# Optimization experiments

Measured on AMD Instinct MI355X. Metric: run time of the kernel, lower is better.

The kernel has to match this reference:

```python
import jax, jax.numpy as jnp
import numpy as np
import math

# Static config (mirrors init_kwargs)
E, B, S, D, F, HMAX = 8, 4, 1024, 1024, 4096, 8
W = 768                      # active slimmable width (multiple giving integer head_dim)
H = max(1, W * HMAX // D)    # = 6 heads at width 768
HD = W // H                  # = 128
TOPK = 2
EPS = 1e-6


def setup_inputs() -> dict:
    key = jax.random.key(0)
    ks = jax.random.split(key, 14)
    sd = 1.0 / math.sqrt(D)
    sf = 1.0 / math.sqrt(F)
    return {
        "x":  jax.random.normal(ks[0], (B, S, D), jnp.float32),
        "wr": jax.random.normal(ks[1], (D, E), jnp.float32) * sd,
        "qw": jax.random.normal(ks[2], (E, D, D), jnp.float32) * sd,
        "qb": jax.random.normal(ks[3], (E, D), jnp.float32) * sd,
        "kw": jax.random.normal(ks[4], (E, D, D), jnp.float32) * sd,
        "kb": jax.random.normal(ks[5], (E, D), jnp.float32) * sd,
        "vw": jax.random.normal(ks[6], (E, D, D), jnp.float32) * sd,
        "vb": jax.random.normal(ks[7], (E, D), jnp.float32) * sd,
        "ow": jax.random.normal(ks[8], (E, D, D), jnp.float32) * sd,
        "ob": jax.random.normal(ks[9], (E, D), jnp.float32) * sd,
        "w1": jax.random.normal(ks[10], (E, F, D), jnp.float32) * sd,
        "b1": jax.random.normal(ks[11], (E, F), jnp.float32) * sd,
        "w2": jax.random.normal(ks[12], (E, D, F), jnp.float32) * sf,
        "b2": jax.random.normal(ks[13], (E, D), jnp.float32) * sf,
    }


def _slim_linear(x, w, b, in_w, out_w):
    # SlimmableLinear: dynamically slice max-size weight/bias to active widths
    return x @ w[:out_w, :in_w].T + b[:out_w]


def _rms_norm(x):
    # SlimmableExpert._layer_norm: RMS normalization (no mean-subtract, no affine)
    var = jnp.mean(jnp.square(x), axis=-1, keepdims=True)
    return x / jnp.sqrt(var + EPS)


def _expert_fwd(x_s, qw, qb, kw, kb, vw, vb, ow, ob, w1, b1, w2, b2):
    # x_s: [B, S, W]  (already sliced to active width)
    # --- slimmable self-attention at width W ---
    q = _slim_linear(x_s, qw, qb, W, W).reshape(B, S, H, HD).transpose(0, 2, 1, 3)
    k = _slim_linear(x_s, kw, kb, W, W).reshape(B, S, H, HD).transpose(0, 2, 1, 3)
    v = _slim_linear(x_s, vw, vb, W, W).reshape(B, S, H, HD).transpose(0, 2, 1, 3)
    scores = jnp.einsum('bhqd,bhkd->bhqk', q, k) / math.sqrt(HD)   # [B,H,S,S]
    attn = jax.nn.softmax(scores, axis=-1)
    ao = jnp.einsum('bhqk,bhkd->bhqd', attn, v)
    ao = ao.transpose(0, 2, 1, 3).reshape(B, S, W)
    ao = _slim_linear(ao, ow, ob, W, W)
    x1 = _rms_norm(x_s + ao)
    # --- slimmable FFN: W -> F (full) -> W, exact GELU (torch default) ---
    h = jax.nn.gelu(_slim_linear(x1, w1, b1, W, F), approximate=False)
    f = _slim_linear(h, w2, b2, F, W)
    return _rms_norm(x1 + f)   # [B,S,W]


def reference(x, wr, qw, qb, kw, kb, vw, vb, ow, ob, w1, b1, w2, b2):
    # Router: softmax over experts, top-k dispatch with renormalized gates
    logits = jnp.einsum('bsd,de->bse', x, wr)            # [B,S,E]
    probs = jax.nn.softmax(logits, axis=-1)
    topv, topi = jax.lax.top_k(probs, TOPK)              # [B,S,K]
    topv = topv / jnp.sum(topv, axis=-1, keepdims=True)
    bi = jnp.arange(B)[:, None, None]
    si = jnp.arange(S)[None, :, None]
    gate = jnp.zeros((B, S, E), x.dtype).at[bi, si, topi].set(topv)  # sparse gate

    # Slice tokens to active width (width embedding skipped: closest stored
    # width 736 != 768, per source shape-match check)
    x_s = x[..., :W]
    outs = []
    for e in range(E):   # small fixed expert count; bounds peak memory
        outs.append(_expert_fwd(x_s, qw[e], qb[e], kw[e], kb[e], vw[e], vb[e],
                                ow[e], ob[e], w1[e], b1[e], w2[e], b2[e]))
    eo = jnp.stack(outs, axis=0)                          # [E,B,S,W]
    out_w = jnp.einsum('bse,ebsw->bsw', gate, eo)         # gate-weighted combine
    # Zero-pad sliced width back to full model dim (per SlimmableExpert)
    out = jnp.concatenate(
        [out_w, jnp.zeros((B, S, D - W), x.dtype)], axis=-1)
    return out
```

## Files before the change

kernel.cpp:

```cpp
#include <hip/hip_runtime.h>
#include <cstdint>

#define NE 8
#define NB 4
#define NS 1024
#define ND 1024
#define NF 4096
#define NW 768
#define NH 6
#define NHD 128
#define NTOK 4096
#define NBH 24
#define RCAP 10496
#define VSTRIDE ((size_t)NTOK * NW)
#define EPS 1e-6f

typedef unsigned short ush;
typedef __attribute__((ext_vector_type(8))) short short8;
typedef __attribute__((ext_vector_type(4))) float f32x4;
typedef __attribute__((ext_vector_type(4))) unsigned short u16x4;

typedef const __attribute__((address_space(1))) void gvoid_t;
typedef __attribute__((address_space(3))) void lvoid_t;

__device__ __forceinline__ void gload16(const void* g, void* l) {
  __builtin_amdgcn_global_load_lds((gvoid_t*)g, (lvoid_t*)l, 16, 0, 0);
}

__device__ __forceinline__ ush f2b(float f) {
  union { float f; uint32_t u; } x; x.f = f;
  uint32_t r = x.u + 0x7fffu + ((x.u >> 16) & 1u);
  return (ush)(r >> 16);
}
__device__ __forceinline__ float b2f(ush u) {
  union { uint32_t u; float f; } x; x.u = (uint32_t)u << 16;
  return x.f;
}
__device__ __forceinline__ int prefix_sum(const int* __restrict__ c, int n) {
  int s = 0;
#pragma unroll 1
  for (int i = 0; i < n; ++i) s += c[i];
  return s;
}


__global__ __launch_bounds__(256, 4)
void router_kernel(const float* __restrict__ x, const float* __restrict__ wr,
                   float* __restrict__ gate, int* __restrict__ inv) {
  int lane = threadIdx.x & 63, wave = threadIdx.x >> 6;
  int t = blockIdx.x * 4 + wave;
  float acc[NE] = {};
  for (int i = 0; i < 16; ++i) {
    int d = lane + i * 64;
    float xv = x[(size_t)t * ND + d];
    const float* wp = wr + (size_t)d * NE;
    float4 w0 = *(const float4*)wp, w1 = *(const float4*)(wp + 4);
    acc[0] += xv * w0.x; acc[1] += xv * w0.y; acc[2] += xv * w0.z; acc[3] += xv * w0.w;
    acc[4] += xv * w1.x; acc[5] += xv * w1.y; acc[6] += xv * w1.z; acc[7] += xv * w1.w;
  }
#pragma unroll
  for (int e = 0; e < NE; ++e)
    for (int m = 1; m < 64; m <<= 1) acc[e] += __shfl_xor(acc[e], m);
  int i1 = 0; float v1 = acc[0];
#pragma unroll
  for (int e = 1; e < NE; ++e) if (acc[e] > v1) { v1 = acc[e]; i1 = e; }
  int i2 = -1; float v2 = -3.0e38f;
#pragma unroll
  for (int e = 0; e < NE; ++e) if (e != i1 && acc[e] > v2) { v2 = acc[e]; i2 = e; }
  float p2 = __expf(v2 - v1);
  float g1 = 1.0f / (1.0f + p2), g2 = p2 / (1.0f + p2);
  if (lane < NE)
    gate[(size_t)t * NE + lane] = (lane == i1) ? g1 : ((lane == i2) ? g2 : 0.0f);
  if (lane < 2) inv[t * 2 + lane] = -1;
}

__global__ __launch_bounds__(1024, 1)
void build_index(const float* __restrict__ gate, int* __restrict__ cnt64s,
                 int* __restrict__ idx_all, int* __restrict__ inv) {
  int e = blockIdx.x >> 2, b = blockIdx.x & 3;
  int s = threadIdx.x, t = b * 1024 + s;
  bool on = gate[(size_t)t * NE + e] > 0.0f;
  idx_all[(e * 4 + b) * 1024 + s] = (b * 1024) | (int)0x80000000;
  __shared__ int wsum[16], wbase[16];
  unsigned long long mask = __ballot(on);
  int lane = s & 63, wv = s >> 6;
  if (lane == 0) wsum[wv] = __popcll(mask);
  __syncthreads();
  if (s == 0) {
    int acc = 0;
    for (int i = 0; i < 16; ++i) { wbase[i] = acc; acc += wsum[i]; }
    cnt64s[e * 4 + b] = (acc + 63) & ~63;
  }
  __syncthreads();
  if (on) {
    int pos = wbase[wv] + __popcll(mask & ((1ull << lane) - 1ull));
    idx_all[(e * 4 + b) * 1024 + pos] = t;
    int k = 0;
#pragma unroll
    for (int j = 0; j < NE; ++j) k += (j < e && gate[(size_t)t * NE + j] > 0.0f);
    inv[t * 2 + k] = (e << 12) | pos;
  }
}

__global__ __launch_bounds__(256, 4)
void cast_all(const float* __restrict__ x,
              const float* __restrict__ qw, const float* __restrict__ kw,
              const float* __restrict__ vw, const float* __restrict__ ow,
              const float* __restrict__ w1, const float* __restrict__ w2,
              ush* __restrict__ xs,
              ush* __restrict__ dq, ush* __restrict__ dk, ush* __restrict__ dv,
              ush* __restrict__ dwo, ush* __restrict__ d1, ush* __restrict__ d2) {
  int y = blockIdx.y;
  if (y == 8) {
    const int n4 = NTOK * NW / 4;
    for (int u = blockIdx.x * 256 + threadIdx.x; u < n4; u += gridDim.x * 256) {
      int r = u / (NW / 4), c = u - r * (NW / 4);
      float4 v = *(const float4*)(x + (size_t)r * ND + c * 4);
      u16x4 o; o.x = f2b(v.x); o.y = f2b(v.y); o.z = f2b(v.z); o.w = f2b(v.w);
      *(u16x4*)(xs + (size_t)u * 4) = o;
    }
    return;
  }
  const int e = y;
  const int Q4 = 147456;
  const int W14 = 786432;
  const int total = 4 * Q4 + 2 * W14;
  const float* qe = qw + (size_t)e * ND * ND;
  const float* ke = kw + (size_t)e * ND * ND;
  const float* ve = vw + (size_t)e * ND * ND;
  const float* oe = ow + (size_t)e * ND * ND;
  const float* w1e = w1 + (size_t)e * NF * ND;
  const float* w2e = w2 + (size_t)e * ND * NF;
  ush* dqe = dq + (size_t)e * NW * NW;
  ush* dke = dk + (size_t)e * NW * NW;
  ush* dve = dv + (size_t)e * NW * NW;
  ush* doe = dwo + (size_t)e * NW * NW;
  ush* d1e = d1 + (size_t)e * NF * NW;
  ush* d2e = d2 + (size_t)e * NW * NF;
  for (int u = blockIdx.x * 256 + threadIdx.x; u < total; u += gridDim.x * 256) {
    const float* src; ush* dst; int ldsrc, cols4, rel;
    if (u < 4 * Q4) {
      int which = u / Q4; rel = u - which * Q4;
      src = (which == 0) ? qe : (which == 1) ? ke : (which == 2) ? ve : oe;
      dst = (which == 0) ? dqe : (which == 1) ? dke : (which == 2) ? dve : doe;
      ldsrc = 1024; cols4 = 192;
    } else if (u < 4 * Q4 + W14) {
      rel = u - 4 * Q4; src = w1e; dst = d1e; ldsrc = 1024; cols4 = 192;
    } else {
      rel = u - 4 * Q4 - W14; src = w2e; dst = d2e; ldsrc = 4096; cols4 = 1024;
    }
    int r = rel / cols4, c = rel - r * cols4;
    float4 v = *(const float4*)(src + (size_t)r * ldsrc + (size_t)c * 4);
    u16x4 o; o.x = f2b(v.x); o.y = f2b(v.y); o.z = f2b(v.z); o.w = f2b(v.w);
    *(u16x4*)(dst + (size_t)rel * 4) = o;
  }
}

#define BM 128
#define BN 128

__device__ __forceinline__ float gelu_fast(float v) {
  float u = v * fmaf(0.0356774081f, v * v, 0.7978845608f);
  float p = __expf(2.0f * fabsf(u));
  float th = fmaf(-2.0f, __builtin_amdgcn_rcpf(p + 1.0f), 1.0f);
  th = copysignf(th, u);
  return 0.5f * v * (1.0f + th);
}

__device__ __forceinline__ void stage_geom2(int tid, int u, int PAIR, int& row, int& kb) {
  row = u + PAIR * (((tid >> 2) ^ (u >> 2)) & 1);
  kb = ((tid ^ u) & 3) << 4;
}

__global__ __launch_bounds__(256, 2)
void qkv_gemm(const ush* __restrict__ A,
              const ush* __restrict__ wqb, const ush* __restrict__ wkb,
              const ush* __restrict__ wvb,
              const float* __restrict__ qbias, const float* __restrict__ kbias,
              const float* __restrict__ vbias,
              ush* __restrict__ qg, ush* __restrict__ kg, ush* __restrict__ vtg,
              const int* __restrict__ cnt64s, const int* __restrict__ idx_all) {
  const int bid = blockIdx.x;
  const int e = bid & 7, wi = bid >> 3;
  const int bn = wi % 3, bm = (wi / 3) % 32, w = wi / 96;
  int sb = 0, cnt = 0;
  if (w == 0) {
    int sec = e * 4 + (bm >> 3);
    cnt = cnt64s[sec];
    if (((bm & 7) * 128) >= cnt) return;
    sb = prefix_sum(cnt64s, sec);
  }
  const ush* Bw = ((w == 0) ? wqb : (w == 1) ? wkb : wvb) + (size_t)e * NW * NW;
  const float* bias = ((w == 0) ? qbias : (w == 1) ? kbias : vbias) + (size_t)e * ND;

  __shared__ __align__(16) char LDS[3 * 24576];

  const int tid = threadIdx.x, lane = tid & 63, wave = tid >> 6;
  const int lr = lane & 15, lg = lane >> 4;
  const int wr = wave >> 1, wc = wave & 1;

  size_t srcOff[6];
#pragma unroll
  for (int c = 0; c < 2; ++c) {
    int u = c * 32 + (tid >> 3), row, kb;
    stage_geom2(tid, u, 64, row, kb);
    int gRow;
    if (w == 0) {
      int lrow = (bm & 7) * 128 + row;
      gRow = idx_all[(e * 4 + (bm >> 3)) * 1024 + lrow] & 0x7fffffff;
    } else {
      gRow = bm * BM + row;
    }
    srcOff[c] = (size_t)gRow * (NW * 2) + kb;
  }
#pragma unroll
  for (int c = 0; c < 4; ++c) {
    int u = c * 32 + (tid >> 3), row, kb;
    stage_geom2(tid, u, 128, row, kb);
    srcOff[2 + c] = (size_t)(bn * 256 + row) * (NW * 2) + kb;
  }

  int offA[4], offB[8];
#pragma unroll
  for (int i = 0; i < 4; ++i)
    offA[i] = (i * 16 + lr) * 128 + (((wr << 6) | (lg << 4)) ^ ((lr & 7) << 4));
#pragma unroll
  for (int j = 0; j < 8; ++j)
    offB[j] = (j * 16 + lr) * 128 + (((wc << 6) | (lg << 4)) ^ ((lr & 7) << 4)) + 8192;

  auto stg = [&](int slot, int kt) {
    size_t kOff = (size_t)kt * 64;
    char* dst = LDS + slot * 24576;
#pragma unroll
    for (int c = 0; c < 2; ++c)
      gload16((const char*)A + srcOff[c] + kOff, dst + c * 4096 + tid * 16);
#pragma unroll
    for (int c = 0; c < 4; ++c)
      gload16((const char*)Bw + srcOff[2 + c] + kOff, dst + 8192 + c * 4096 + tid * 16);
  };

  f32x4 acc[4][8] = {};
  const int nkt = NW / 32;
  stg(0, 0); stg(1, 1);
  asm volatile("s_waitcnt vmcnt(6)" ::: "memory");
  asm volatile("s_barrier" ::: "memory");
  int slot = 0;
  for (int kt = 0; kt < nkt; ++kt) {
    int s2 = slot + 2; if (s2 >= 3) s2 -= 3;
    bool more = (kt + 2 < nkt);
    if (more) stg(s2, kt + 2);
    const char* base = LDS + slot * 24576;
    short8 af[4], bfr[8];
#pragma unroll
    for (int i = 0; i < 4; ++i) af[i] = *(const short8*)(base + offA[i]);
#pragma unroll
    for (int j = 0; j < 8; ++j) bfr[j] = *(const short8*)(base + offB[j]);
    __builtin_amdgcn_s_setprio(1);
#pragma unroll
    for (int i = 0; i < 4; ++i)
#pragma unroll
      for (int j = 0; j < 8; ++j)
        acc[i][j] = __builtin_amdgcn_mfma_f32_16x16x32_bf16(af[i], bfr[j], acc[i][j], 0, 0, 0);
    __builtin_amdgcn_s_setprio(0);
    if (more) asm volatile("s_waitcnt vmcnt(6)" ::: "memory");
    else      asm volatile("s_waitcnt vmcnt(0)" ::: "memory");
    asm volatile("s_barrier" ::: "memory");
    slot = (slot == 2) ? 0 : slot + 1;
  }

#pragma unroll
  for (int i = 0; i < 4; ++i) {
    int lm16 = (bm & 7) * 128 + wr * 64 + i * 16;
    int m0 = bm * BM + wr * 64 + i * 16 + lg * 4;
#pragma unroll
    for (int j = 0; j < 8; ++j) {
      int n = bn * 256 + wc * 128 + j * 16 + lr;
      float bb = bias[n];
      if (w == 0) {
        if (lm16 < cnt) {
          int grow = sb + lm16 + lg * 4;
#pragma unroll
          for (int r = 0; r < 4; ++r)
            qg[(size_t)(grow + r) * NW + n] = f2b(acc[i][j][r] + bb);
        }
      } else if (w == 1) {
        ush* o = kg + (size_t)e * NTOK * NW;
#pragma unroll
        for (int r = 0; r < 4; ++r)
          o[(size_t)(m0 + r) * NW + n] = f2b(acc[i][j][r] + bb);
      } else {
        int b_ = m0 >> 10, s0 = m0 & 1023, h_ = n >> 7, d = n & 127;
        u16x4 wv_;
#pragma unroll
        for (int r = 0; r < 4; ++r) wv_[r] = f2b(acc[i][j][r] + bb);
        *(u16x4*)(vtg + (size_t)e * VSTRIDE +
                  ((size_t)(b_ * NH + h_) * NHD + d) * NS + s0) = wv_;
      }
    }
  }
}

__global__ __launch_bounds__(256, 3)
void attn2(const ush* __restrict__ Qg, const ush* __restrict__ Kg,
           const ush* __restrict__ VTg,
           ush* __restrict__ po, float* __restrict__ mlm, float* __restrict__ mll,
           const int* __restrict__ cnt64s) {
  const int bid = blockIdx.x;
  const int e = bid & 7, wi = bid >> 3;
  const int qb = wi & 15, yy = wi >> 4;
  const int bh = yy >> 1, half = yy & 1;
  const int b = bh / NH, h = bh % NH;
  const int sec = e * 4 + b;
  const int cnt = cnt64s[sec];
  if (qb * 64 >= cnt) return;
  const int sb = prefix_sum(cnt64s, sec);

  __shared__ __align__(16) ush Ks[64 * 128];
  __shared__ __align__(16) ush VTs[128 * 64];
  __shared__ __align__(16) ush Ps[4 * 16 * 64];

  const int tid = threadIdx.x, lane = tid & 63, wave = tid >> 6;
  const int lr = lane & 15, lg = lane >> 4;
  const int k0 = half * 512;
  const float cexp = 1.4426950408889634f / sqrtf((float)NHD);

  const ush* Ke = Kg + (size_t)e * NTOK * NW;
  const ush* Ve = VTg + (size_t)e * VSTRIDE;

  int growq = sb + qb * 64 + wave * 16 + lr;
  short8 qf[4];
#pragma unroll
  for (int kk = 0; kk < 4; ++kk)
    qf[kk] = *(const short8*)(Qg + (size_t)growq * NW + h * NHD + kk * 32 + lg * 8);

  f32x4 accv[8] = {};
  float mr[4] = {-3.0e38f, -3.0e38f, -3.0e38f, -3.0e38f};
  float ls[4] = {};

  for (int kt = 0; kt < 8; ++kt) {
    __syncthreads();
#pragma unroll
    for (int p = 0; p < 4; ++p) {
      int o = p * 4096 + tid * 16;
      int row = o >> 8, cb = o & 255;
      gload16((const char*)Ke + ((size_t)(b * NS + k0 + kt * 64 + row) * NW + h * NHD) * 2 +
                  (cb ^ ((row & 7) << 4)),
              (char*)Ks + o);
    }
#pragma unroll
    for (int p = 0; p < 4; ++p) {
      int o = p * 4096 + tid * 16;
      int d = o >> 7, cb = o & 127;
      gload16((const char*)Ve + ((size_t)((b * NH + h) * NHD + d) * NS + k0 + kt * 64) * 2 +
                  (cb ^ ((d & 7) << 4)),
              (char*)VTs + o);
    }
    __syncthreads();

    f32x4 s[4] = {};
    __builtin_amdgcn_s_setprio(1);
#pragma unroll
    for (int kg2 = 0; kg2 < 4; ++kg2)
#pragma unroll
      for (int kk = 0; kk < 4; ++kk) {
        int row = kg2 * 16 + lr;
        short8 kf = *(const short8*)((const char*)Ks + row * 256 +
                                     ((kk * 64 + lg * 16) ^ ((row & 7) << 4)));
        s[kg2] = __builtin_amdgcn_mfma_f32_16x16x32_bf16(qf[kk], kf, s[kg2], 0, 0, 0);
      }
    __builtin_amdgcn_s_setprio(0);

    float mt[4];
#pragma unroll
    for (int r = 0; r < 4; ++r) {
      float m0 = fmaxf(fmaxf(s[0][r], s[1][r]), fmaxf(s[2][r], s[3][r]));
#pragma unroll
      for (int mm = 1; mm < 16; mm <<= 1) m0 = fmaxf(m0, __shfl_xor(m0, mm));
      mt[r] = m0;
    }
    bool need = (mt[0] > mr[0] + 8.f) || (mt[1] > mr[1] + 8.f) ||
                (mt[2] > mr[2] + 8.f) || (mt[3] > mr[3] + 8.f);
    if (__any(need)) {
#pragma unroll
      for (int r = 0; r < 4; ++r) {
        float mn = fmaxf(mr[r], mt[r]);
        float sc = exp2f((mr[r] - mn) * cexp);
        mr[r] = mn; ls[r] *= sc;
#pragma unroll
        for (int dg = 0; dg < 8; ++dg) accv[dg][r] *= sc;
      }
    }

    char* pw = (char*)Ps + wave * 2048;
#pragma unroll
    for (int kg2 = 0; kg2 < 4; ++kg2)
#pragma unroll
      for (int r = 0; r < 4; ++r) {
        float p = exp2f((s[kg2][r] - mr[r]) * cexp);
        ls[r] += p;
        int row = lg * 4 + r;
        *(ush*)(pw + row * 128 + (((kg2 * 16 + lr) * 2) ^ ((row & 7) << 4))) = f2b(p);
      }
    short8 pf[2];
#pragma unroll
    for (int kk2 = 0; kk2 < 2; ++kk2)
      pf[kk2] = *(const short8*)(pw + lr * 128 + ((kk2 * 64 + lg * 16) ^ ((lr & 7) << 4)));

    __builtin_amdgcn_s_setprio(1);
#pragma unroll
    for (int dg = 0; dg < 8; ++dg) {
      int d = dg * 16 + lr;
#pragma unroll
      for (int kk2 = 0; kk2 < 2; ++kk2) {
        short8 vf = *(const short8*)((const char*)VTs + d * 128 +
                                     ((kk2 * 64 + lg * 16) ^ ((d & 7) << 4)));
        accv[dg] = __builtin_amdgcn_mfma_f32_16x16x32_bf16(pf[kk2], vf, accv[dg], 0, 0, 0);
      }
    }
    __builtin_amdgcn_s_setprio(0);
  }

#pragma unroll
  for (int r = 0; r < 4; ++r)
#pragma unroll
    for (int mm = 1; mm < 16; mm <<= 1) ls[r] += __shfl_xor(ls[r], mm);

#pragma unroll
  for (int r = 0; r < 4; ++r) {
    int growr = sb + qb * 64 + wave * 16 + lg * 4 + r;
#pragma unroll
    for (int dg = 0; dg < 8; ++dg)
      po[((size_t)(growr * NH + h) * 2 + half) * NHD + dg * 16 + lr] = f2b(accv[dg][r]);
  }
  if (lr == 0) {
#pragma unroll
    for (int r = 0; r < 4; ++r) {
      int growr = sb + qb * 64 + wave * 16 + lg * 4 + r;
      mlm[(size_t)(growr * NH + h) * 2 + half] = mr[r];
      mll[(size_t)(growr * NH + h) * 2 + half] = ls[r];
    }
  }
}

__global__ __launch_bounds__(256, 4)
void attn_combine(const ush* __restrict__ po, const float* __restrict__ mlm,
                  const float* __restrict__ mll, ush* __restrict__ ao,
                  const int* __restrict__ cnt64s) {
  const float cexp = 1.4426950408889634f / sqrtf((float)NHD);
  int Rtot = prefix_sum(cnt64s, 32);
  int idx = blockIdx.x * 256 + threadIdx.x;
  int row = idx >> 4, dq = idx & 15;
  int grow = row / NH, h = row - grow * NH;
  if (grow >= Rtot) return;
  float m[2], l[2], M = -3.0e38f;
#pragma unroll
  for (int hh = 0; hh < 2; ++hh) {
    m[hh] = mlm[(size_t)row * 2 + hh];
    l[hh] = mll[(size_t)row * 2 + hh];
    M = fmaxf(M, m[hh]);
  }
  float L = 0.0f, w[2];
#pragma unroll
  for (int hh = 0; hh < 2; ++hh) { w[hh] = exp2f((m[hh] - M) * cexp); L += l[hh] * w[hh]; }
  float inv_ = 1.0f / L;
  float o[8] = {};
#pragma unroll
  for (int hh = 0; hh < 2; ++hh) {
    short8 v = *(const short8*)(po + ((size_t)row * 2 + hh) * NHD + dq * 8);
#pragma unroll
    for (int j = 0; j < 8; ++j) o[j] += b2f((ush)v[j]) * w[hh];
  }
  short8 res;
#pragma unroll
  for (int j = 0; j < 8; ++j) res[j] = (short)f2b(o[j] * inv_);
  *(short8*)(ao + (size_t)grow * NW + h * NHD + dq * 8) = res;
}

__global__ __launch_bounds__(256, 2)
void csr_gemm_w(const ush* __restrict__ A, const ush* __restrict__ Ball,
                const float* __restrict__ biasAll, ush* __restrict__ out,
                int N, int Kld, int klen, int nbn,
                int strideBe, int biasStride,
                const int* __restrict__ cnt64s) {
  const int bid = blockIdx.x;
  const int e = bid & 7, wi = bid >> 3;
  const int bn = wi % nbn, bm = wi / nbn;
  const int Re = cnt64s[e * 4] + cnt64s[e * 4 + 1] + cnt64s[e * 4 + 2] + cnt64s[e * 4 + 3];
  if (bm * BM >= Re) return;
  const int ebase = prefix_sum(cnt64s, e * 4);
  const ush* Bw = Ball + (size_t)e * strideBe;
  const float* bias = biasAll + (size_t)e * biasStride;

  __shared__ __align__(16) char LDS[3 * 24576];

  const int tid = threadIdx.x, lane = tid & 63, wave = tid >> 6;
  const int lr = lane & 15, lg = lane >> 4;
  const int wr = wave >> 1, wc = wave & 1;

  size_t srcOff[6];
#pragma unroll
  for (int c = 0; c < 2; ++c) {
    int u = c * 32 + (tid >> 3), row, kb;
    stage_geom2(tid, u, 64, row, kb);
    srcOff[c] = (size_t)(ebase + bm * BM + row) * (Kld * 2) + kb;
  }
#pragma unroll
  for (int c = 0; c < 4; ++c) {
    int u = c * 32 + (tid >> 3), row, kb;
    stage_geom2(tid, u, 128, row, kb);
    srcOff[2 + c] = (size_t)(bn * 256 + row) * (Kld * 2) + kb;
  }

  int offA[4], offB[8];
#pragma unroll
  for (int i = 0; i < 4; ++i)
    offA[i] = (i * 16 + lr) * 128 + (((wr << 6) | (lg << 4)) ^ ((lr & 7) << 4));
#pragma unroll
  for (int j = 0; j < 8; ++j)
    offB[j] = (j * 16 + lr) * 128 + (((wc << 6) | (lg << 4)) ^ ((lr & 7) << 4)) + 8192;

  auto stg = [&](int slot, int kt) {
    size_t kOff = (size_t)kt * 64;
    char* dst = LDS + slot * 24576;
#pragma unroll
    for (int c = 0; c < 2; ++c)
      gload16((const char*)A + srcOff[c] + kOff, dst + c * 4096 + tid * 16);
#pragma unroll
    for (int c = 0; c < 4; ++c)
      gload16((const char*)Bw + srcOff[2 + c] + kOff, dst + 8192 + c * 4096 + tid * 16);
  };

  f32x4 acc[4][8] = {};
  const int nkt = klen / 32;
  stg(0, 0); stg(1, 1);
  asm volatile("s_waitcnt vmcnt(6)" ::: "memory");
  asm volatile("s_barrier" ::: "memory");
  int slot = 0;
  for (int kt = 0; kt < nkt; ++kt) {
    int s2 = slot + 2; if (s2 >= 3) s2 -= 3;
    bool more = (kt + 2 < nkt);
    if (more) stg(s2, kt + 2);
    const char* base = LDS + slot * 24576;
    short8 af[4], bfr[8];
#pragma unroll
    for (int i = 0; i < 4; ++i) af[i] = *(const short8*)(base + offA[i]);
#pragma unroll
    for (int j = 0; j < 8; ++j) bfr[j] = *(const short8*)(base + offB[j]);
    __builtin_amdgcn_s_setprio(1);
#pragma unroll
    for (int i = 0; i < 4; ++i)
#pragma unroll
      for (int j = 0; j < 8; ++j)
        acc[i][j] = __builtin_amdgcn_mfma_f32_16x16x32_bf16(af[i], bfr[j], acc[i][j], 0, 0, 0);
    __builtin_amdgcn_s_setprio(0);
    if (more) asm volatile("s_waitcnt vmcnt(6)" ::: "memory");
    else      asm volatile("s_waitcnt vmcnt(0)" ::: "memory");
    asm volatile("s_barrier" ::: "memory");
    slot = (slot == 2) ? 0 : slot + 1;
  }

#pragma unroll
  for (int i = 0; i < 4; ++i) {
    int lm16 = bm * BM + wr * 64 + i * 16;
    if (lm16 >= Re) continue;
#pragma unroll
    for (int j = 0; j < 8; ++j) {
      int n = bn * 256 + wc * 128 + j * 16 + lr;
      float bb = bias[n];
      int row0 = ebase + lm16 + lg * 4;
#pragma unroll
      for (int r = 0; r < 4; ++r)
        out[(size_t)(row0 + r) * N + n] = f2b(gelu_fast(acc[i][j][r] + bb));
    }
  }
}

template <int EPI>
__global__ __launch_bounds__(256, 3)
void csr_gemm(const ush* __restrict__ A, const ush* __restrict__ Ball,
              const float* __restrict__ biasAll, ush* __restrict__ out,
              int N, int Kld, int klen, int nbn, int nbm, int nsplit,
              int strideBe, int biasStride,
              const int* __restrict__ cnt64s) {
  const int bid = blockIdx.x;
  const int e = bid & 7, wi = bid >> 3;
  const int bn = wi % nbn, bm = (wi / nbn) % nbm, s = wi / (nbn * nbm);
  const int Re = cnt64s[e * 4] + cnt64s[e * 4 + 1] + cnt64s[e * 4 + 2] + cnt64s[e * 4 + 3];
  if (bm * BM >= Re) return;
  const int ebase = prefix_sum(cnt64s, e * 4);
  const ush* Bw = Ball + (size_t)e * strideBe;
  const float* bias = (s == 0) ? biasAll + (size_t)e * biasStride : nullptr;
  const int koff = s * klen;
  ush* outp = out + (size_t)s * RCAP * N;

  __shared__ __align__(16) char LDS[3 * 16384];

  const int tid = threadIdx.x, lane = tid & 63, wave = tid >> 6;
  const int lr = lane & 15, lg = lane >> 4;
  const int wr = wave >> 1, wc = wave & 1;

  size_t srcOff[4];
#pragma unroll
  for (int c = 0; c < 4; ++c) {
    int u = (c & 1) * 32 + (tid >> 3), row, kb;
    stage_geom2(tid, u, 64, row, kb);
    int gRow = (c < 2) ? (ebase + bm * BM + row) : (bn * BN + row);
    srcOff[c] = (size_t)gRow * (Kld * 2) + (size_t)koff * 2 + kb;
  }

  int offA[4], offB[4];
#pragma unroll
  for (int i = 0; i < 4; ++i) {
    offA[i] = (i * 16 + lr) * 128 + (((wr << 6) | (lg << 4)) ^ ((lr & 7) << 4));
    offB[i] = (i * 16 + lr) * 128 + (((wc << 6) | (lg << 4)) ^ ((lr & 7) << 4)) + 8192;
  }

  auto stg = [&](int slot, int kt) {
    size_t kOff = (size_t)kt * 64;
    char* dst = LDS + slot * 16384;
#pragma unroll
    for (int c = 0; c < 4; ++c) {
      const char* src = (c < 2) ? (const char*)A + srcOff[c] + kOff
                                : (const char*)Bw + srcOff[c] + kOff;
      gload16(src, dst + c * 4096 + tid * 16);
    }
  };

  f32x4 acc[4][4] = {};
  const int nkt = klen / 32;
  stg(0, 0); stg(1, 1);
  asm volatile("s_waitcnt vmcnt(4)" ::: "memory");
  asm volatile("s_barrier" ::: "memory");
  int slot = 0;
  for (int kt = 0; kt < nkt; ++kt) {
    int s2 = slot + 2; if (s2 >= 3) s2 -= 3;
    bool more = (kt + 2 < nkt);
    if (more) stg(s2, kt + 2);
    const char* base = LDS + slot * 16384;
    short8 af[4], bfr[4];
#pragma unroll
    for (int i = 0; i < 4; ++i) {
      af[i] = *(const short8*)(base + offA[i]);
      bfr[i] = *(const short8*)(base + offB[i]);
    }
    __builtin_amdgcn_s_setprio(1);
#pragma unroll
    for (int i = 0; i < 4; ++i)
#pragma unroll
      for (int j = 0; j < 4; ++j)
        acc[i][j] = __builtin_amdgcn_mfma_f32_16x16x32_bf16(af[i], bfr[j], acc[i][j], 0, 0, 0);
    __builtin_amdgcn_s_setprio(0);
    if (more) asm volatile("s_waitcnt vmcnt(4)" ::: "memory");
    else      asm volatile("s_waitcnt vmcnt(0)" ::: "memory");
    asm volatile("s_barrier" ::: "memory");
    slot = (slot == 2) ? 0 : slot + 1;
  }

#pragma unroll
  for (int i = 0; i < 4; ++i) {
    int lm16 = bm * BM + wr * 64 + i * 16;
    if (lm16 >= Re) continue;
#pragma unroll
    for (int j = 0; j < 4; ++j) {
      int n = bn * BN + wc * 64 + j * 16 + lr;
      float bb = bias ? bias[n] : 0.0f;
      int row0 = ebase + lm16 + lg * 4;
#pragma unroll
      for (int r = 0; r < 4; ++r)
        outp[(size_t)(row0 + r) * N + n] = f2b(acc[i][j][r] + bb);
    }
  }
}

__global__ __launch_bounds__(256, 4)
void rmsnorm_res(const float* __restrict__ x, const ush* __restrict__ ooP,
                 ush* __restrict__ x1b, const int* __restrict__ cnt64s,
                 const int* __restrict__ idx_all) {
  int r = blockIdx.x;
  int base = 0, sec = -1, loc = 0;
#pragma unroll 1
  for (int i = 0; i < 32; ++i) {
    int cc = cnt64s[i];
    if (sec < 0 && r < base + cc) { sec = i; loc = r - base; }
    base += cc;
  }
  if (sec < 0) return;
  int t = idx_all[sec * 1024 + loc] & 0x7fffffff;
  __shared__ float red[4];
  int c = threadIdx.x, lane = c & 63, wave = c >> 6;
  float v[3]; float ss = 0.0f;
#pragma unroll
  for (int i = 0; i < 3; ++i) {
    int col = c + i * 256;
    float a = x[(size_t)t * ND + col] + b2f(ooP[(size_t)r * NW + col]) +
              b2f(ooP[(size_t)RCAP * NW + (size_t)r * NW + col]);
    v[i] = a; ss += a * a;
  }
#pragma unroll
  for (int m = 1; m < 64; m <<= 1) ss += __shfl_xor(ss, m);
  if (lane == 0) red[wave] = ss;
  __syncthreads();
  float tot = red[0] + red[1] + red[2] + red[3];
  float scale = rsqrtf(tot / (float)NW + EPS);
#pragma unroll
  for (int i = 0; i < 3; ++i) {
    int col = c + i * 256;
    x1b[(size_t)r * NW + col] = f2b(v[i] * scale);
  }
}

__global__ __launch_bounds__(256, 4)
void final_token(const ush* __restrict__ x1b, const ush* __restrict__ ffp,
                 const float* __restrict__ gate, const int* __restrict__ inv,
                 const int* __restrict__ cnt64s, float* __restrict__ out) {
  int t = blockIdx.x, c = threadIdx.x, lane = c & 63, wave = c >> 6;
  __shared__ float red[4];
  float acc[3] = {0.0f, 0.0f, 0.0f};
#pragma unroll 1
  for (int k = 0; k < 2; ++k) {
    int v = inv[t * 2 + k];
    if (v >= 0) {
      int e = v >> 12, pos = v & 0xfff;
      int b = t >> 10;
      int grow = prefix_sum(cnt64s, e * 4 + b) + pos;
      float g = gate[(size_t)t * NE + e];
      float vv[3]; float ss = 0.0f;
#pragma unroll
      for (int i = 0; i < 3; ++i) {
        int col = c + i * 256;
        float f = b2f(ffp[(size_t)grow * NW + col]) +
                  b2f(ffp[(size_t)RCAP * NW + (size_t)grow * NW + col]) +
                  b2f(ffp[2 * (size_t)RCAP * NW + (size_t)grow * NW + col]) +
                  b2f(ffp[3 * (size_t)RCAP * NW + (size_t)grow * NW + col]);
        float a = b2f(x1b[(size_t)grow * NW + col]) + f;
        vv[i] = a; ss += a * a;
      }
#pragma unroll
      for (int m = 1; m < 64; m <<= 1) ss += __shfl_xor(ss, m);
      if (lane == 0) red[wave] = ss;
      __syncthreads();
      float tot = red[0] + red[1] + red[2] + red[3];
      float scale = rsqrtf(tot / (float)NW + EPS) * g;
#pragma unroll
      for (int i = 0; i < 3; ++i) acc[i] += vv[i] * scale;
      __syncthreads();
    }
  }
#pragma unroll
  for (int i = 0; i < 3; ++i) out[(size_t)t * ND + c + i * 256] = acc[i];
  out[(size_t)t * ND + 768 + c] = 0.0f;
}

extern "C" void kernel_launch(void* const* d_in, const int* in_sizes, int n_in,
                              void* d_out, int out_size, void* d_ws, size_t ws_size,
                              hipStream_t stream) {
  (void)in_sizes; (void)n_in; (void)ws_size; (void)out_size;
  const float* x  = (const float*)d_in[0];
  const float* wr = (const float*)d_in[1];
  const float* qw = (const float*)d_in[2];
  const float* qbias = (const float*)d_in[3];
  const float* kw = (const float*)d_in[4];
  const float* kbias = (const float*)d_in[5];
  const float* vw = (const float*)d_in[6];
  const float* vbias = (const float*)d_in[7];
  const float* ow = (const float*)d_in[8];
  const float* obias = (const float*)d_in[9];
  const float* w1 = (const float*)d_in[10];
  const float* b1 = (const float*)d_in[11];
  const float* w2 = (const float*)d_in[12];
  const float* b2 = (const float*)d_in[13];
  float* out = (float*)d_out;
  char* ws = (char*)d_ws;

  size_t off = 0;
  auto alloc = [&](size_t bytes) {
    void* p = ws + off;
    off += (bytes + 255) & ~(size_t)255;
    return p;
  };
  float* gate = (float*)alloc((size_t)NTOK * NE * 4);
  int* cnt64s = (int*)alloc(32 * 4);
  int* idx_all = (int*)alloc((size_t)NE * NTOK * 4);
  int* inv = (int*)alloc((size_t)NTOK * 2 * 4);
  ush* xs  = (ush*)alloc((size_t)NTOK * NW * 2);
  ush* wqb = (ush*)alloc((size_t)NE * NW * NW * 2);
  ush* wkb = (ush*)alloc((size_t)NE * NW * NW * 2);
  ush* wvb = (ush*)alloc((size_t)NE * NW * NW * 2);
  ush* wob = (ush*)alloc((size_t)NE * NW * NW * 2);
  ush* w1b = (ush*)alloc((size_t)NE * NF * NW * 2);
  ush* w2b = (ush*)alloc((size_t)NE * NW * NF * 2);
  ush* x1b = (ush*)alloc((size_t)RCAP * NW * 2);
  char* arena1 = (char*)alloc((size_t)RCAP * NF * 2);
  ush* qg  = (ush*)arena1;
  ush* po  = (ush*)(arena1 + 16121856);
  float* mlm = (float*)(arena1 + 80609280);
  float* mll = (float*)(arena1 + 81616896);
  ush* hb  = (ush*)arena1;
  char* arena2 = (char*)alloc(112852992);
  ush* kg  = (ush*)arena2;
  ush* vtg = (ush*)(arena2 + 50331648);
  ush* aog = (ush*)arena2;
  ush* ooP = (ush*)(arena2 + 16121856);
  ush* ffp = (ush*)(arena2 + 48365568);

  router_kernel<<<dim3(NTOK / 4), 256, 0, stream>>>(x, wr, gate, inv);
  build_index<<<dim3(NE * NB), 1024, 0, stream>>>(gate, cnt64s, idx_all, inv);
  cast_all<<<dim3(288, 9), 256, 0, stream>>>(x, qw, kw, vw, ow, w1, w2,
                                             xs, wqb, wkb, wvb, wob, w1b, w2b);

  qkv_gemm<<<dim3(8 * 288), 256, 0, stream>>>(
      xs, wqb, wkb, wvb, qbias, kbias, vbias, qg, kg, vtg, cnt64s, idx_all);

  attn2<<<dim3(8 * 768), 256, 0, stream>>>(qg, kg, vtg, po, mlm, mll, cnt64s);
  attn_combine<<<dim3(RCAP * NH * 16 / 256), 256, 0, stream>>>(po, mlm, mll, aog, cnt64s);

  csr_gemm<0><<<dim3(8 * 384), 256, 0, stream>>>(
      aog, wob, obias, ooP, NW, NW, 384, 6, 32, 2, NW * NW, ND, cnt64s);

  rmsnorm_res<<<dim3(RCAP), 256, 0, stream>>>(x, ooP, x1b, cnt64s, idx_all);

  csr_gemm_w<<<dim3(8 * 512), 256, 0, stream>>>(
      x1b, w1b, b1, hb, NF, NW, NW, 16, NF * NW, NF, cnt64s);

  csr_gemm<0><<<dim3(8 * 768), 256, 0, stream>>>(
      hb, w2b, b2, ffp, NW, NF, 1024, 6, 32, 4, NW * NF, ND, cnt64s);

  final_token<<<dim3(NTOK), 256, 0, stream>>>(x1b, ffp, gate, inv, cnt64s, out);
}
```

Baseline: 586.0 us.

## Retune work splits: smaller QKV tiles, single-pass attention, fewer split-K partitions

The QKV GEMM moves from 128x256 tiles to 128x128 tiles, doubling the grid and allowing three blocks per CU through smaller LDS use. Attention no longer splits the key range in two, so the attn_combine kernel and its partial-output traffic go away and each block normalizes and writes its output directly. The output projection drops split-K (from two partitions to one) and the FFN down projection goes from four partitions to two, which cuts partial-sum writes and reads in rmsnorm_res and final_token. The trade is less parallelism per launch and longer serial loops per block, which could leave CUs underfilled.

Measured after the change: 565.2 us. 3.6% less time.

```diff
diff --git a/kernel.cpp b/kernel.cpp
--- a/kernel.cpp
+++ b/kernel.cpp
@@ -172,7 +172,7 @@
   kb = ((tid ^ u) & 3) << 4;
 }
 
-__global__ __launch_bounds__(256, 2)
+__global__ __launch_bounds__(256, 3)
 void qkv_gemm(const ush* __restrict__ A,
               const ush* __restrict__ wqb, const ush* __restrict__ wkb,
               const ush* __restrict__ wvb,
@@ -182,7 +182,7 @@
               const int* __restrict__ cnt64s, const int* __restrict__ idx_all) {
   const int bid = blockIdx.x;
   const int e = bid & 7, wi = bid >> 3;
-  const int bn = wi % 3, bm = (wi / 3) % 32, w = wi / 96;
+  const int bn = wi % 6, bm = (wi / 6) % 32, w = wi / 192;
   int sb = 0, cnt = 0;
   if (w == 0) {
     int sec = e * 4 + (bm >> 3);
@@ -193,76 +193,74 @@
   const ush* Bw = ((w == 0) ? wqb : (w == 1) ? wkb : wvb) + (size_t)e * NW * NW;
   const float* bias = ((w == 0) ? qbias : (w == 1) ? kbias : vbias) + (size_t)e * ND;
 
-  __shared__ __align__(16) char LDS[3 * 24576];
+  __shared__ __align__(16) char LDS[3 * 16384];
 
   const int tid = threadIdx.x, lane = tid & 63, wave = tid >> 6;
   const int lr = lane & 15, lg = lane >> 4;
   const int wr = wave >> 1, wc = wave & 1;
 
-  size_t srcOff[6];
-#pragma unroll
-  for (int c = 0; c < 2; ++c) {
-    int u = c * 32 + (tid >> 3), row, kb;
+  size_t srcOff[4];
+#pragma unroll
+  for (int c = 0; c < 4; ++c) {
+    int u = (c & 1) * 32 + (tid >> 3), row, kb;
     stage_geom2(tid, u, 64, row, kb);
     int gRow;
-    if (w == 0) {
-      int lrow = (bm & 7) * 128 + row;
-      gRow = idx_all[(e * 4 + (bm >> 3)) * 1024 + lrow] & 0x7fffffff;
+    if (c < 2) {
+      if (w == 0) {
+        int lrow = (bm & 7) * 128 + row;
+        gRow = idx_all[(e * 4 + (bm >> 3)) * 1024 + lrow] & 0x7fffffff;
+      } else {
+        gRow = bm * BM + row;
+      }
     } else {
-      gRow = bm * BM + row;
+      gRow = bn * BN + row;
     }
     srcOff[c] = (size_t)gRow * (NW * 2) + kb;
   }
-#pragma unroll
-  for (int c = 0; c < 4; ++c) {
-    int u = c * 32 + (tid >> 3), row, kb;
-    stage_geom2(tid, u, 128, row, kb);
-    srcOff[2 + c] = (size_t)(bn * 256 + row) * (NW * 2) + kb;
-  }
-
-  int offA[4], offB[8];
-#pragma unroll
-  for (int i = 0; i < 4; ++i)
+
+  int offA[4], offB[4];
+#pragma unroll
+  for (int i = 0; i < 4; ++i) {
     offA[i] = (i * 16 + lr) * 128 + (((wr << 6) | (lg << 4)) ^ ((lr & 7) << 4));
-#pragma unroll
-  for (int j = 0; j < 8; ++j)
-    offB[j] = (j * 16 + lr) * 128 + (((wc << 6) | (lg << 4)) ^ ((lr & 7) << 4)) + 8192;
+    offB[i] = (i * 16 + lr) * 128 + (((wc << 6) | (lg << 4)) ^ ((lr & 7) << 4)) + 8192;
+  }
 
   auto stg = [&](int slot, int kt) {
     size_t kOff = (size_t)kt * 64;
-    char* dst = LDS + slot * 24576;
-#pragma unroll
-    for (int c = 0; c < 2; ++c)
-      gload16((const char*)A + srcOff[c] + kOff, dst + c * 4096 + tid * 16);
-#pragma unroll
-    for (int c = 0; c < 4; ++c)
-      gload16((const char*)Bw + srcOff[2 + c] + kOff, dst + 8192 + c * 4096 + tid * 16);
+    char* dst = LDS + slot * 16384;
+#pragma unroll
+    for (int c = 0; c < 4; ++c) {
+      const char* src = (c < 2) ? (const char*)A + srcOff[c] + kOff
+                                : (const char*)Bw + srcOff[c] + kOff;
+      gload16(src, dst + c * 4096 + tid * 16);
+    }
   };
 
-  f32x4 acc[4][8] = {};
+  f32x4 acc[4][4] = {};
   const int nkt = NW / 32;
   stg(0, 0); stg(1, 1);
-  asm volatile("s_waitcnt vmcnt(6)" ::: "memory");
+  asm volatile("s_waitcnt vmcnt(4)" ::: "memory");
   asm volatile("s_barrier" ::: "memory");
   int slot = 0;
   for (int kt = 0; kt < nkt; ++kt) {
     int s2 = slot + 2; if (s2 >= 3) s2 -= 3;
     bool more = (kt + 2 < nkt);
     if (more) stg(s2, kt + 2);
-    const char* base = LDS + slot * 24576;
-    short8 af[4], bfr[8];
-#pragma unroll
-    for (int i = 0; i < 4; ++i) af[i] = *(const short8*)(base + offA[i]);
-#pragma unroll
-    for (int j = 0; j < 8; ++j) bfr[j] = *(const short8*)(base + offB[j]);
+    const char* base = LDS + slot * 16384;
+    short8 af[4], bfr[4];
+#pragma unroll
+    for (int i = 0; i < 4; ++i) {
+      af[i] = *(const short8*)(base + offA[i]);
+      bfr[i] = *(const short8*)(base + offB[i]);
+    }
     __builtin_amdgcn_s_setprio(1);
 #pragma unroll
     for (int i = 0; i < 4; ++i)
 #pragma unroll
-      for (int j = 0; j < 8; ++j)
+      for (int j = 0; j < 4; ++j)
         acc[i][j] = __builtin_amdgcn_mfma_f32_16x16x32_bf16(af[i], bfr[j], acc[i][j], 0, 0, 0);
     __builtin_amdgcn_s_setprio(0);
-    if (more) asm volatile("s_waitcnt vmcnt(6)" ::: "memory");
+    if (more) asm volatile("s_waitcnt vmcnt(4)" ::: "memory");
     else      asm volatile("s_waitcnt vmcnt(0)" ::: "memory");
     asm volatile("s_barrier" ::: "memory");
     slot = (slot == 2) ? 0 : slot + 1;
@@ -273,8 +271,8 @@
     int lm16 = (bm & 7) * 128 + wr * 64 + i * 16;
     int m0 = bm * BM + wr * 64 + i * 16 + lg * 4;
 #pragma unroll
-    for (int j = 0; j < 8; ++j) {
-      int n = bn * 256 + wc * 128 + j * 16 + lr;
+    for (int j = 0; j < 4; ++j) {
+      int n = bn * BN + wc * 64 + j * 16 + lr;
       float bb = bias[n];
       if (w == 0) {
         if (lm16 < cnt) {
@@ -302,13 +300,11 @@
 
 __global__ __launch_bounds__(256, 3)
 void attn2(const ush* __restrict__ Qg, const ush* __restrict__ Kg,
-           const ush* __restrict__ VTg,
-           ush* __restrict__ po, float* __restrict__ mlm, float* __restrict__ mll,
+           const ush* __restrict__ VTg, ush* __restrict__ ao,
            const int* __restrict__ cnt64s) {
   const int bid = blockIdx.x;
   const int e = bid & 7, wi = bid >> 3;
-  const int qb = wi & 15, yy = wi >> 4;
-  const int bh = yy >> 1, half = yy & 1;
+  const int qb = wi & 15, bh = wi >> 4;
   const int b = bh / NH, h = bh % NH;
   const int sec = e * 4 + b;
   const int cnt = cnt64s[sec];
@@ -321,7 +317,6 @@
 
   const int tid = threadIdx.x, lane = tid & 63, wave = tid >> 6;
   const int lr = lane & 15, lg = lane >> 4;
-  const int k0 = half * 512;
   const float cexp = 1.4426950408889634f / sqrtf((float)NHD);
 
   const ush* Ke = Kg + (size_t)e * NTOK * NW;
@@ -337,13 +332,13 @@
   float mr[4] = {-3.0e38f, -3.0e38f, -3.0e38f, -3.0e38f};
   float ls[4] = {};
 
-  for (int kt = 0; kt < 8; ++kt) {
+  for (int kt = 0; kt < 16; ++kt) {
     __syncthreads();
 #pragma unroll
     for (int p = 0; p < 4; ++p) {
       int o = p * 4096 + tid * 16;
       int row = o >> 8, cb = o & 255;
-      gload16((const char*)Ke + ((size_t)(b * NS + k0 + kt * 64 + row) * NW + h * NHD) * 2 +
+      gload16((const char*)Ke + ((size_t)(b * NS + kt * 64 + row) * NW + h * NHD) * 2 +
                   (cb ^ ((row & 7) << 4)),
               (char*)Ks + o);
     }
@@ -351,7 +346,7 @@
     for (int p = 0; p < 4; ++p) {
       int o = p * 4096 + tid * 16;
       int d = o >> 7, cb = o & 127;
-      gload16((const char*)Ve + ((size_t)((b * NH + h) * NHD + d) * NS + k0 + kt * 64) * 2 +
+      gload16((const char*)Ve + ((size_t)((b * NH + h) * NHD + d) * NS + kt * 64) * 2 +
                   (cb ^ ((d & 7) << 4)),
               (char*)VTs + o);
     }
@@ -428,52 +423,11 @@
 #pragma unroll
   for (int r = 0; r < 4; ++r) {
     int growr = sb + qb * 64 + wave * 16 + lg * 4 + r;
+    float inv_ = 1.0f / ls[r];
 #pragma unroll
     for (int dg = 0; dg < 8; ++dg)
-      po[((size_t)(growr * NH + h) * 2 + half) * NHD + dg * 16 + lr] = f2b(accv[dg][r]);
-  }
-  if (lr == 0) {
-#pragma unroll
-    for (int r = 0; r < 4; ++r) {
-      int growr = sb + qb * 64 + wave * 16 + lg * 4 + r;
-      mlm[(size_t)(growr * NH + h) * 2 + half] = mr[r];
-      mll[(size_t)(growr * NH + h) * 2 + half] = ls[r];
-    }
-  }
-}
-
-__global__ __launch_bounds__(256, 4)
-void attn_combine(const ush* __restrict__ po, const float* __restrict__ mlm,
-                  const float* __restrict__ mll, ush* __restrict__ ao,
-                  const int* __restrict__ cnt64s) {
-  const float cexp = 1.4426950408889634f / sqrtf((float)NHD);
-  int Rtot = prefix_sum(cnt64s, 32);
-  int idx = blockIdx.x * 256 + threadIdx.x;
-  int row = idx >> 4, dq = idx & 15;
-  int grow = row / NH, h = row - grow * NH;
-  if (grow >= Rtot) return;
-  float m[2], l[2], M = -3.0e38f;
-#pragma unroll
-  for (int hh = 0; hh < 2; ++hh) {
-    m[hh] = mlm[(size_t)row * 2 + hh];
-    l[hh] = mll[(size_t)row * 2 + hh];
-    M = fmaxf(M, m[hh]);
-  }
-  float L = 0.0f, w[2];
-#pragma unroll
-  for (int hh = 0; hh < 2; ++hh) { w[hh] = exp2f((m[hh] - M) * cexp); L += l[hh] * w[hh]; }
-  float inv_ = 1.0f / L;
-  float o[8] = {};
-#pragma unroll
-  for (int hh = 0; hh < 2; ++hh) {
-    short8 v = *(const short8*)(po + ((size_t)row * 2 + hh) * NHD + dq * 8);
-#pragma unroll
-    for (int j = 0; j < 8; ++j) o[j] += b2f((ush)v[j]) * w[hh];
-  }
-  short8 res;
-#pragma unroll
-  for (int j = 0; j < 8; ++j) res[j] = (short)f2b(o[j] * inv_);
-  *(short8*)(ao + (size_t)grow * NW + h * NHD + dq * 8) = res;
+      ao[(size_t)growr * NW + h * NHD + dg * 16 + lr] = f2b(accv[dg][r] * inv_);
+  }
 }
 
 __global__ __launch_bounds__(256, 2)
@@ -575,7 +529,6 @@
   }
 }
 
-template <int EPI>
 __global__ __launch_bounds__(256, 3)
 void csr_gemm(const ush* __restrict__ A, const ush* __restrict__ Ball,
               const float* __restrict__ biasAll, ush* __restrict__ out,
@@ -692,8 +645,7 @@
 #pragma unroll
   for (int i = 0; i < 3; ++i) {
     int col = c + i * 256;
-    float a = x[(size_t)t * ND + col] + b2f(ooP[(size_t)r * NW + col]) +
-              b2f(ooP[(size_t)RCAP * NW + (size_t)r * NW + col]);
+    float a = x[(size_t)t * ND + col] + b2f(ooP[(size_t)r * NW + col]);
     v[i] = a; ss += a * a;
   }
 #pragma unroll
@@ -729,9 +681,7 @@
       for (int i = 0; i < 3; ++i) {
         int col = c + i * 256;
         float f = b2f(ffp[(size_t)grow * NW + col]) +
-                  b2f(ffp[(size_t)RCAP * NW + (size_t)grow * NW + col]) +
-                  b2f(ffp[2 * (size_t)RCAP * NW + (size_t)grow * NW + col]) +
-                  b2f(ffp[3 * (size_t)RCAP * NW + (size_t)grow * NW + col]);
+                  b2f(ffp[(size_t)RCAP * NW + (size_t)grow * NW + col]);
         float a = b2f(x1b[(size_t)grow * NW + col]) + f;
         vv[i] = a; ss += a * a;
       }
@@ -792,38 +742,34 @@
   ush* x1b = (ush*)alloc((size_t)RCAP * NW * 2);
   char* arena1 = (char*)alloc((size_t)RCAP * NF * 2);
   ush* qg  = (ush*)arena1;
-  ush* po  = (ush*)(arena1 + 16121856);
-  float* mlm = (float*)(arena1 + 80609280);
-  float* mll = (float*)(arena1 + 81616896);
+  ush* aog = (ush*)(arena1 + 16121856);
   ush* hb  = (ush*)arena1;
   char* arena2 = (char*)alloc(112852992);
   ush* kg  = (ush*)arena2;
   ush* vtg = (ush*)(arena2 + 50331648);
-  ush* aog = (ush*)arena2;
   ush* ooP = (ush*)(arena2 + 16121856);
-  ush* ffp = (ush*)(arena2 + 48365568);
+  ush* ffp = (ush*)(arena2 + 32243712);
 
   router_kernel<<<dim3(NTOK / 4), 256, 0, stream>>>(x, wr, gate, inv);
   build_index<<<dim3(NE * NB), 1024, 0, stream>>>(gate, cnt64s, idx_all, inv);
   cast_all<<<dim3(288, 9), 256, 0, stream>>>(x, qw, kw, vw, ow, w1, w2,
                                              xs, wqb, wkb, wvb, wob, w1b, w2b);
 
-  qkv_gemm<<<dim3(8 * 288), 256, 0, stream>>>(
+  qkv_gemm<<<dim3(8 * 576), 256, 0, stream>>>(
       xs, wqb, wkb, wvb, qbias, kbias, vbias, qg, kg, vtg, cnt64s, idx_all);
 
-  attn2<<<dim3(8 * 768), 256, 0, stream>>>(qg, kg, vtg, po, mlm, mll, cnt64s);
-  attn_combine<<<dim3(RCAP * NH * 16 / 256), 256, 0, stream>>>(po, mlm, mll, aog, cnt64s);
-
-  csr_gemm<0><<<dim3(8 * 384), 256, 0, stream>>>(
-      aog, wob, obias, ooP, NW, NW, 384, 6, 32, 2, NW * NW, ND, cnt64s);
+  attn2<<<dim3(8 * 384), 256, 0, stream>>>(qg, kg, vtg, aog, cnt64s);
+
+  csr_gemm<<<dim3(8 * 192), 256, 0, stream>>>(
+      aog, wob, obias, ooP, NW, NW, NW, 6, 32, 1, NW * NW, ND, cnt64s);
 
   rmsnorm_res<<<dim3(RCAP), 256, 0, stream>>>(x, ooP, x1b, cnt64s, idx_all);
 
   csr_gemm_w<<<dim3(8 * 512), 256, 0, stream>>>(
       x1b, w1b, b1, hb, NF, NW, NW, 16, NF * NW, NF, cnt64s);
 
-  csr_gemm<0><<<dim3(8 * 768), 256, 0, stream>>>(
-      hb, w2b, b2, ffp, NW, NF, 1024, 6, 32, 4, NW * NF, ND, cnt64s);
+  csr_gemm<<<dim3(8 * 384), 256, 0, stream>>>(
+      hb, w2b, b2, ffp, NW, NF, 2048, 6, 32, 2, NW * NF, ND, cnt64s);
 
   final_token<<<dim3(NTOK), 256, 0, stream>>>(x1b, ffp, gate, inv, cnt64s, out);
 }
```
